# Kernel optimization log

Hardware: AMD Instinct MI355X
Metric: run time of the kernel (lower is better)

Reference implementation:

```python
import jax, jax.numpy as jnp
import numpy as np

BATCH, D_IN, D_HIDDEN, K = 4096, 2048, 16384, 64


def setup_inputs() -> dict:
    key = jax.random.key(0)
    kx, kw = jax.random.split(key)
    x = jax.random.normal(kx, (BATCH, D_IN), dtype=jnp.float32)
    # W init as in the module: randn normalized per column (dim=0) then scaled by 0.1
    W = jax.random.normal(kw, (D_IN, D_HIDDEN), dtype=jnp.float32)
    W = 0.1 * W / jnp.linalg.norm(W, axis=0, keepdims=True)
    b_enc = jnp.zeros((D_HIDDEN,), dtype=jnp.float32)
    b_dec = jnp.zeros((D_IN,), dtype=jnp.float32)
    return {"x": x, "W": W, "b_enc": b_enc, "b_dec": b_dec, "k": K}


def reference(x, W, b_enc, b_dec, k):
    # encode: linear + ReLU
    f = jax.nn.relu(x @ W + b_enc)            # [B, D_HIDDEN]
    # global batch top-k: keep k * batch largest activations across the whole batch
    flat = f.reshape(-1)                      # [B * D_HIDDEN]
    n_keep = k * x.shape[0]                   # static python int
    vals, idx = jax.lax.top_k(flat, n_keep)
    f_topk = jnp.zeros_like(flat).at[idx].set(vals).reshape(f.shape)
    # tied decode
    recon = f_topk @ W.T + b_dec              # [B, D_IN]
    return (recon, f_topk)
```

## Files before the change

### kernel.cpp

```cpp
#include <hip/hip_runtime.h>
#include <stdint.h>


#define BATCH 4096
#define DIN   2048
#define DHID  16384
#define NELEM (BATCH * DHID)
#define RECON_ELEMS (BATCH * DIN)
#define NBINS 8192
#define THRESH_BIN 1664
#define SC_THRESH 0.203125f
#define WIN   3
#define RLCAP 256
#define CBUF2 512
#define NB2 (NBINS - THRESH_BIN)
#define NB2H (NB2 / 2)
#define SCHUNK 32
#define NCH ((NB2 + SCHUNK - 1) / SCHUNK)
#define NKT 32
#define SBUF8 4096
#define WSCALE_INV 0.00390625f

#define XB_OFF   0u
#define HIST_OFF 16777216u
#define META_OFF (HIST_OFF + 32768u)
#define CAND_OFF (HIST_OFF + 65536u)
#define CANDCAP  80000u
#define SC_OFF   18874368u
#define SCCAP    1835008u

#define M_CNT   0
#define M_BLO   1
#define M_BHI   2
#define M_NNEED 3
#define M_NSURE 4
#define M_OVF   5
#define M_SCCNT 6

struct Cand { unsigned long long key; unsigned int idx; float val; };

typedef _Float16 f16x8 __attribute__((ext_vector_type(8)));
typedef float f32x4  __attribute__((ext_vector_type(4)));

__device__ __forceinline__ int binof(float v) {
    int b = (int)(v * 8192.0f);
    return b > (NBINS - 1) ? (NBINS - 1) : b;
}

__device__ __forceinline__ unsigned short f2h(float f) {
    _Float16 h = (_Float16)f;
    return __builtin_bit_cast(unsigned short, h);
}

__device__ __forceinline__ float h2f(unsigned short u) {
    return (float)__builtin_bit_cast(_Float16, u);
}

__device__ __forceinline__ void gload_lds16(const void* g, void* l) {
    __builtin_amdgcn_global_load_lds(
        (const __attribute__((address_space(1))) void*)g,
        (__attribute__((address_space(3))) void*)l, 16, 0, 0);
}

__device__ __forceinline__ void nt_store4(const float4& v, float* p) {
    f32x4 x = {v.x, v.y, v.z, v.w};
    __builtin_nontemporal_store(x, (f32x4*)p);
}

__global__ void init_kernel(unsigned* __restrict__ hist, unsigned* __restrict__ meta) {
    int i = blockIdx.x * 256 + threadIdx.x;
    if (i < NBINS) hist[i] = 0u;
    if (i < 64)    meta[i] = 0u;
}

__global__ __launch_bounds__(256) void convert_x_init(const float* __restrict__ X,
                                                      unsigned short* __restrict__ Xh,
                                                      unsigned* __restrict__ hist,
                                                      unsigned* __restrict__ meta,
                                                      unsigned* __restrict__ rowcnt) {
    const int bid = blockIdx.x;
    size_t i = (size_t)bid * 256 + threadIdx.x;
    float4 v = ((const float4*)X)[i];
    ushort4 o;
    o.x = f2h(v.x); o.y = f2h(v.y); o.z = f2h(v.z); o.w = f2h(v.w);
    ((ushort4*)Xh)[i] = o;
    if (bid < 32) {
        int g = bid * 256 + threadIdx.x;
        if (g < NBINS)  hist[g] = 0u;
        if (g < 64)     meta[g] = 0u;
        if (g < BATCH)  rowcnt[g] = 0u;
    }
}

__global__ __launch_bounds__(256) void transpose_both(const float* __restrict__ W,
                                                      float* __restrict__ WT,
                                                      unsigned short* __restrict__ WhT) {
    __shared__ float tile[64][68];
    const int t  = threadIdx.x;
    const int gx = blockIdx.x;
    const int gy = blockIdx.y;
    const int ra = t >> 4;
    const int ca = (t & 15) * 4;
#pragma unroll
    for (int u = 0; u < 4; ++u) {
        int row = u * 16 + ra;
        float4 v = *(const float4*)&W[(size_t)(gy * 64 + row) * DHID + gx * 64 + ca];
        tile[ca + 0][row] = v.x;
        tile[ca + 1][row] = v.y;
        tile[ca + 2][row] = v.z;
        tile[ca + 3][row] = v.w;
    }
    __syncthreads();
#pragma unroll
    for (int u = 0; u < 4; ++u) {
        int cl = u * 16 + ra;
        float4 v = *(const float4*)&tile[cl][ca];
        size_t o = (size_t)(gx * 64 + cl) * DIN + gy * 64 + ca;
        *(float4*)&WT[o] = v;
        ushort4 b;
        b.x = f2h(v.x * 256.0f); b.y = f2h(v.y * 256.0f);
        b.z = f2h(v.z * 256.0f); b.w = f2h(v.w * 256.0f);
        *(ushort4*)&WhT[o] = b;
    }
}


#define STAGE_A(H, KT) do { if ((KT) < NKT) {                                   \
    const unsigned short* _s = Xh + (size_t)(m0 + (H)*128 + stgrow)*2048        \
                               + (KT)*64 + stgcol;                              \
    unsigned short* _d = lds + ((H)*2 + ((KT)&1))*8192 + stgdst;                \
    gload_lds16(_s, _d);                                                        \
    gload_lds16(_s + 64*2048, _d + 4096);                                       \
} } while (0)

#define STAGE_B(H, KT) do { if ((KT) < NKT) {                                   \
    const unsigned short* _s = WhT + (size_t)(n0 + (H)*128 + stgrow)*2048       \
                               + (KT)*64 + stgcol;                              \
    unsigned short* _d = lds + 32768 + ((H)*2 + ((KT)&1))*8192 + stgdst;        \
    gload_lds16(_s, _d);                                                        \
    gload_lds16(_s + 64*2048, _d + 4096);                                       \
} } while (0)

#define PHASE(Q, PAR, AH, BH, ...) do {                                         \
    f16x8 av[4][2], bv[2][2];                                                   \
    _Pragma("unroll")                                                           \
    for (int i = 0; i < 4; ++i) {                                               \
        const unsigned short* _p = lds + ((AH)*2+(PAR))*8192                    \
                                   + (wr2*64 + i*16 + lm)*64;                   \
        av[i][0] = *(const f16x8*)(_p + cs0);                                   \
        av[i][1] = *(const f16x8*)(_p + cs1);                                   \
    }                                                                           \
    _Pragma("unroll")                                                           \
    for (int j = 0; j < 2; ++j) {                                               \
        const unsigned short* _p = lds + 32768 + ((BH)*2+(PAR))*8192            \
                                   + (wn*32 + j*16 + lm)*64;                    \
        bv[j][0] = *(const f16x8*)(_p + cs0);                                   \
        bv[j][1] = *(const f16x8*)(_p + cs1);                                   \
    }                                                                           \
    __VA_ARGS__                                                                 \
    __builtin_amdgcn_s_barrier();                                               \
    asm volatile("s_waitcnt lgkmcnt(0)" ::: "memory");                          \
    __builtin_amdgcn_sched_barrier(0);                                          \
    __builtin_amdgcn_s_setprio(1);                                              \
    _Pragma("unroll")                                                           \
    for (int i = 0; i < 4; ++i)                                                 \
    _Pragma("unroll")                                                           \
    for (int j = 0; j < 2; ++j) {                                               \
        acc[Q][i][j] = __builtin_amdgcn_mfma_f32_16x16x32_f16(                  \
            av[i][0], bv[j][0], acc[Q][i][j], 0, 0, 0);                         \
        acc[Q][i][j] = __builtin_amdgcn_mfma_f32_16x16x32_f16(                  \
            av[i][1], bv[j][1], acc[Q][i][j], 0, 0, 0);                         \
    }                                                                           \
    __builtin_amdgcn_s_setprio(0);                                              \
    __builtin_amdgcn_s_barrier();                                               \
    asm volatile("" ::: "memory");                                              \
} while (0)

__global__ __launch_bounds__(512, 2) void encode_mfma8(const unsigned short* __restrict__ Xh,
                                                       const unsigned short* __restrict__ WhT,
                                                       const float* __restrict__ benc,
                                                       unsigned long long* __restrict__ sc,
                                                       unsigned* __restrict__ meta,
                                                       unsigned* __restrict__ hist,
                                                       float* __restrict__ F) {
    __shared__ unsigned short lds[65536];
    __shared__ unsigned hsh[NB2H];
    __shared__ unsigned s_n, s_base;

    const int t   = threadIdx.x;
    const int wid = t >> 6;
    const int l   = t & 63;
    const int wr2 = wid >> 2;
    const int wn  = wid & 3;
    const int lm  = l & 15;
    const int l7  = l & 7;
    const int cs0 = ((l >> 4) * 8) ^ (l7 * 8);
    const int cs1 = cs0 ^ 32;
    const int stgrow = wid * 8 + (l >> 3);
    const int stgcol = (l7 ^ (l >> 3)) * 8;
    const int stgdst = wid * 512;

    if (t == 0) s_n = 0u;
    for (int i2 = t; i2 < NB2H; i2 += 512) hsh[i2] = 0u;

    const unsigned id  = blockIdx.x;
    const unsigned xcd = id & 7u;
    const unsigned c   = id >> 3;
    const int bx = (int)(xcd * 8u + (c & 7u));
    const int by = (int)(c >> 3);
    const int m0 = by * 256;
    const int n0 = bx * 256;

    f32x4 acc[4][4][2];
#pragma unroll
    for (int q = 0; q < 4; ++q)
#pragma unroll
        for (int i = 0; i < 4; ++i)
#pragma unroll
            for (int j = 0; j < 2; ++j) acc[q][i][j] = (f32x4){0.f, 0.f, 0.f, 0.f};

    STAGE_A(0, 0); STAGE_B(0, 0); STAGE_B(1, 0); STAGE_A(1, 0);
    STAGE_A(0, 1); STAGE_B(1, 1);
    asm volatile("s_waitcnt vmcnt(4)" ::: "memory");
    __builtin_amdgcn_s_barrier();
    asm volatile("" ::: "memory");

#pragma unroll 1
    for (int it = 0; it < 16; ++it) {
        const int T = 2 * it;
        PHASE(0, 0, 0, 0, STAGE_B(0, T + 1); STAGE_A(1, T + 1););
        PHASE(1, 0, 0, 1, (void)0;);
        PHASE(2, 0, 1, 1, STAGE_A(0, T + 2););
        PHASE(3, 0, 1, 0, STAGE_B(1, T + 2);
                          asm volatile("s_waitcnt vmcnt(4)" ::: "memory"););
        PHASE(0, 1, 0, 0, STAGE_B(0, T + 2); STAGE_A(1, T + 2););
        PHASE(1, 1, 0, 1, (void)0;);
        PHASE(2, 1, 1, 1, STAGE_A(0, T + 3););
        PHASE(3, 1, 1, 0, STAGE_B(1, T + 3);
                          asm volatile("s_waitcnt vmcnt(4)" ::: "memory"););
    }

    __syncthreads();
    unsigned long long* sbuf = (unsigned long long*)lds;

#pragma unroll
    for (int q = 0; q < 4; ++q) {
        const int qm = (q >= 2) ? 1 : 0;
        const int qn = (q == 1 || q == 2) ? 1 : 0;
#pragma unroll
        for (int j = 0; j < 2; ++j) {
            const int col = n0 + qn * 128 + wn * 32 + j * 16 + lm;
            const float bias = benc[col];
#pragma unroll
            for (int i = 0; i < 4; ++i) {
                const int rbase = m0 + qm * 128 + wr2 * 64 + i * 16 + (l >> 4) * 4;
#pragma unroll
                for (int r = 0; r < 4; ++r) {
                    float v = fmaxf(acc[q][i][j][r] * WSCALE_INV + bias, 0.0f);
                    if (v >= SC_THRESH) {
                        unsigned hx = (unsigned)(binof(v) - THRESH_BIN);
                        atomicAdd(&hsh[hx >> 1], (hx & 1u) ? 65536u : 1u);
                        unsigned flat = (unsigned)(rbase + r) * (unsigned)DHID + (unsigned)col;
                        unsigned long long e =
                            ((unsigned long long)__float_as_uint(v) << 32) | flat;
                        unsigned pos = atomicAdd(&s_n, 1u);
                        if (pos < SBUF8) sbuf[pos] = e;
                        else {
                            unsigned p = atomicAdd(&meta[M_SCCNT], 1u);
                            if (p < SCCAP) sc[p] = e; else meta[M_OVF] = 1u;
                        }
                    }
                }
            }
        }
    }
    {
        const float4 z4 = {0.f, 0.f, 0.f, 0.f};
        const int zr = t >> 6;
        const int zc = (t & 63) * 4;
#pragma unroll 1
        for (int rr = 0; rr < 32; ++rr)
            nt_store4(z4, &F[(size_t)(m0 + zr + rr * 8) * DHID + n0 + zc]);
    }
    __syncthreads();
    unsigned n = s_n < SBUF8 ? s_n : (unsigned)SBUF8;
    if (t == 0) s_base = atomicAdd(&meta[M_SCCNT], n);
    __syncthreads();
    const unsigned base = s_base;
    for (unsigned l2 = t; l2 < n; l2 += 512) {
        unsigned p = base + l2;
        if (p < SCCAP) sc[p] = sbuf[l2]; else meta[M_OVF] = 1u;
    }
    for (int i2 = t; i2 < NB2H; i2 += 512) {
        unsigned u = hsh[i2];
        unsigned lo = u & 0xFFFFu, hi = u >> 16;
        if (lo) atomicAdd(&hist[THRESH_BIN + 2 * i2], lo);
        if (hi) atomicAdd(&hist[THRESH_BIN + 2 * i2 + 1], hi);
    }
}

__global__ void scan_sc(const unsigned* __restrict__ hist,
                        unsigned* __restrict__ meta,
                        const int* __restrict__ kptr) {
    __shared__ unsigned sh[NB2];
    __shared__ unsigned csum[NCH];
    int t = threadIdx.x;
    for (int i = t; i < NB2; i += 256) sh[i] = hist[THRESH_BIN + i];
    __syncthreads();
    if (t < NCH) {
        unsigned s = 0;
        int base = t * SCHUNK;
        for (int u = 0; u < SCHUNK && base + u < NB2; ++u) s += sh[base + u];
        csum[t] = s;
    }
    __syncthreads();
    if (t == 0) {
        unsigned nk = (unsigned)kptr[0] * BATCH;
        unsigned cum = 0;
        int bstar_idx = -1;
        for (int c = NCH - 1; c >= 0; --c) {
            if (cum + csum[c] >= nk) {
                int hi2 = c * SCHUNK + SCHUNK - 1; if (hi2 >= NB2) hi2 = NB2 - 1;
                for (int idx = hi2; idx >= c * SCHUNK; --idx) {
                    cum += sh[idx];
                    if (cum >= nk) { bstar_idx = idx; break; }
                }
                break;
            } else cum += csum[c];
        }
        if (bstar_idx < 0) { meta[M_OVF] = 2u; bstar_idx = WIN; }
        int bstar = THRESH_BIN + bstar_idx;
        int blo = bstar - WIN;
        if (blo < THRESH_BIN) { meta[M_OVF] = 3u; blo = THRESH_BIN; }
        int bhi = bstar + WIN; if (bhi > NBINS - 1) bhi = NBINS - 1;
        int bhi_idx = bhi - THRESH_BIN;
        unsigned nsure = 0;
        int cstart = (bhi_idx + 1 + SCHUNK - 1) / SCHUNK;
        for (int idx = bhi_idx + 1; idx < cstart * SCHUNK && idx < NB2; ++idx) nsure += sh[idx];
        for (int c = cstart; c < NCH; ++c) nsure += csum[c];
        meta[M_BLO]   = (unsigned)blo;
        meta[M_BHI]   = (unsigned)bhi;
        meta[M_NSURE] = nsure;
        meta[M_NNEED] = nk - nsure;
    }
}

__global__ __launch_bounds__(256) void emit_sc(const unsigned long long* __restrict__ sc,
                                               unsigned* __restrict__ meta,
                                               Cand* __restrict__ cand,
                                               unsigned* __restrict__ rowcnt,
                                               unsigned long long* __restrict__ rowlist) {
    __shared__ uint2 s_cand[CBUF2];
    __shared__ unsigned s_nc, s_base;
    const int tid = threadIdx.x;
    if (tid == 0) s_nc = 0u;
    __syncthreads();
    const unsigned blo = meta[M_BLO], bhi = meta[M_BHI];
    unsigned C = meta[M_SCCNT]; if (C > SCCAP) C = SCCAP;
    size_t stride = (size_t)gridDim.x * 256;
    for (size_t i = (size_t)blockIdx.x * 256 + tid; i < C; i += stride) {
        unsigned long long e = sc[i];
        unsigned vbits = (unsigned)(e >> 32);
        unsigned idx   = (unsigned)(e & 0xFFFFFFFFu);
        unsigned b = (unsigned)binof(__uint_as_float(vbits));
        if (b > bhi) {
            unsigned row = idx >> 14;
            unsigned pos = atomicAdd(&rowcnt[row], 1u);
            if (pos < RLCAP)
                rowlist[(size_t)row * RLCAP + pos] =
                    ((unsigned long long)vbits << 32) | (idx & (DHID - 1));
            else meta[M_OVF] = 1u;
        } else if (b >= blo) {
            unsigned pos = atomicAdd(&s_nc, 1u);
            if (pos < CBUF2) { s_cand[pos].x = idx; s_cand[pos].y = vbits; }
            else {
                unsigned p = atomicAdd(&meta[M_CNT], 1u);
                if (p < CANDCAP) { cand[p].idx = idx; cand[p].val = __uint_as_float(vbits); }
                else meta[M_OVF] = 1u;
            }
        }
    }
    __syncthreads();
    unsigned nc = s_nc < CBUF2 ? s_nc : (unsigned)CBUF2;
    if (tid == 0) s_base = atomicAdd(&meta[M_CNT], nc);
    __syncthreads();
    const unsigned base = s_base;
    for (unsigned l2 = tid; l2 < nc; l2 += 256) {
        unsigned p = base + l2;
        if (p < CANDCAP) { cand[p].idx = s_cand[l2].x; cand[p].val = __uint_as_float(s_cand[l2].y); }
        else meta[M_OVF] = 1u;
    }
}

__global__ __launch_bounds__(64) void scatter_rl(const unsigned long long* __restrict__ rowlist,
                                                 const unsigned* __restrict__ rowcnt,
                                                 float* __restrict__ F) {
    int b = blockIdx.x;
    unsigned cnt = rowcnt[b]; if (cnt > RLCAP) cnt = RLCAP;
    for (unsigned l = threadIdx.x; l < cnt; l += 64) {
        unsigned long long e = rowlist[(size_t)b * RLCAP + l];
        unsigned j = (unsigned)(e & 0xFFFFFFFFu);
        F[(size_t)b * DHID + j] = __uint_as_float((unsigned)(e >> 32));
    }
}

__global__ __launch_bounds__(256) void exact_wave(const float* __restrict__ X,
                                                  const float* __restrict__ WT,
                                                  const float* __restrict__ benc,
                                                  const unsigned* __restrict__ meta,
                                                  Cand* __restrict__ cand) {
    unsigned C = meta[M_CNT]; if (C > CANDCAP) C = CANDCAP;
    const int lane = threadIdx.x & 63;
    const unsigned wid = blockIdx.x * 4 + (threadIdx.x >> 6);
    const unsigned nw  = gridDim.x * 4;
    for (unsigned c = wid * 2; c < C; c += nw * 2) {
        unsigned c1 = c + 1;
        bool has1 = (c1 < C);
        unsigned idxA = cand[c].idx;
        unsigned idxB = cand[has1 ? c1 : c].idx;
        const float4* xA = (const float4*)(X  + (size_t)(idxA >> 14) * DIN);
        const float4* wA = (const float4*)(WT + (size_t)(idxA & (DHID - 1)) * DIN);
        const float4* xB = (const float4*)(X  + (size_t)(idxB >> 14) * DIN);
        const float4* wB = (const float4*)(WT + (size_t)(idxB & (DHID - 1)) * DIN);
        double a0 = 0.0, a1 = 0.0;
#pragma unroll
        for (int u = 0; u < 8; ++u) {
            float4 xa = xA[lane + 64 * u];
            float4 wa = wA[lane + 64 * u];
            float4 xb = xB[lane + 64 * u];
            float4 wb = wB[lane + 64 * u];
            a0 += (double)xa.x * (double)wa.x + (double)xa.y * (double)wa.y
                + (double)xa.z * (double)wa.z + (double)xa.w * (double)wa.w;
            a1 += (double)xb.x * (double)wb.x + (double)xb.y * (double)wb.y
                + (double)xb.z * (double)wb.z + (double)xb.w * (double)wb.w;
        }
#pragma unroll
        for (int off = 32; off > 0; off >>= 1) {
            a0 += __shfl_down(a0, off, 64);
            a1 += __shfl_down(a1, off, 64);
        }
        if (lane == 0) {
            double v0 = a0 + (double)benc[idxA & (DHID - 1)];
            if (v0 < 0.0) v0 = 0.0;
            cand[c].key = (unsigned long long)__double_as_longlong(v0);
            if (has1) {
                double v1 = a1 + (double)benc[idxB & (DHID - 1)];
                if (v1 < 0.0) v1 = 0.0;
                cand[c1].key = (unsigned long long)__double_as_longlong(v1);
            }
        }
    }
}

__global__ __launch_bounds__(1024) void select_kernel(unsigned* __restrict__ meta,
                                                      Cand* __restrict__ cand) {
    __shared__ unsigned h[4096];
    __shared__ unsigned csum[128];
    __shared__ unsigned long long s_prefix;
    __shared__ unsigned s_need, s_gcnt;
    __shared__ unsigned long long gkey[1024];
    __shared__ unsigned gpos[1024];
    __shared__ unsigned gidx[1024];
    __shared__ unsigned char gkeep[1024];

    int t = threadIdx.x;
    unsigned C = meta[M_CNT]; if (C > CANDCAP) C = CANDCAP;
    if (t == 0) { s_prefix = 0ULL; s_need = meta[M_NNEED]; s_gcnt = 0u; }
    __syncthreads();

    for (int pass = 0; pass < 3; ++pass) {
        for (int i = t; i < 4096; i += 1024) h[i] = 0u;
        __syncthreads();
        int shift = 52 - pass * 12;
        unsigned long long pfx = s_prefix;
        for (unsigned c = t; c < C; c += 1024) {
            unsigned long long key = cand[c].key;
            if (pass == 0 || (key >> (shift + 12)) == pfx)
                atomicAdd(&h[(unsigned)((key >> shift) & 0xFFFULL)], 1u);
        }
        __syncthreads();
        if (t < 128) {
            unsigned s = 0;
#pragma unroll
            for (int u = 0; u < 32; ++u) s += h[t * 32 + u];
            csum[t] = s;
        }
        __syncthreads();
        if (t == 0) {
            unsigned need = s_need;
            unsigned cum2 = 0; int cc = 127;
            for (; cc >= 0; --cc) {
                if (cum2 + csum[cc] >= need) break;
                cum2 += csum[cc];
            }
            int bsel = 0;
            if (cc >= 0) {
                unsigned cum3 = cum2;
                for (int b = cc * 32 + 31; b >= cc * 32; --b) {
                    cum3 += h[b];
                    if (cum3 >= need) { bsel = b; s_need = need - (cum3 - h[b]); break; }
                }
            }
            s_prefix = (s_prefix << 12) | (unsigned long long)bsel;
        }
        __syncthreads();
    }
    unsigned long long pfx = s_prefix;
    for (unsigned c = t; c < C; c += 1024) {
        unsigned long long key = cand[c].key;
        if ((key >> 28) == pfx) {
            unsigned p = atomicAdd(&s_gcnt, 1u);
            if (p < 1024) { gkey[p] = key; gpos[p] = c; gidx[p] = cand[c].idx; gkeep[p] = 0; }
        }
    }
    __syncthreads();
    if (t == 0) {
        unsigned g = s_gcnt < 1024u ? s_gcnt : 1024u;
        unsigned nd = s_need;
        for (unsigned sel = 0; sel < nd && sel < g; ++sel) {
            int best = -1;
            for (unsigned i = 0; i < g; ++i) {
                if (gkeep[i]) continue;
                if (best < 0 || gkey[i] > gkey[best] ||
                    (gkey[i] == gkey[best] && gidx[i] < gidx[best])) best = (int)i;
            }
            if (best >= 0) gkeep[best] = 1;
        }
        for (unsigned i = 0; i < g; ++i)
            if (gkeep[i]) cand[gpos[i]].idx = gidx[i] | 0x80000000u;
    }
    __syncthreads();
    for (unsigned c = t; c < C; c += 1024)
        if ((cand[c].key >> 28) > pfx) cand[c].idx |= 0x80000000u;
}

__global__ __launch_bounds__(256) void restore2_kernel(float* __restrict__ F,
                                                       const unsigned* __restrict__ meta,
                                                       const Cand* __restrict__ cand,
                                                       unsigned* __restrict__ rowcnt,
                                                       unsigned long long* __restrict__ rowlist) {
    unsigned C = meta[M_CNT]; if (C > CANDCAP) C = CANDCAP;
    size_t stride = (size_t)gridDim.x * 256;
    for (size_t c = (size_t)blockIdx.x * 256 + threadIdx.x; c < C; c += stride) {
        unsigned id = cand[c].idx;
        if (id & 0x80000000u) {
            unsigned idx = id & 0x7FFFFFFFu;
            float v = (float)__longlong_as_double((long long)cand[c].key);
            F[idx] = v;
            unsigned row = idx >> 14;
            unsigned j   = idx & (DHID - 1);
            unsigned pos = atomicAdd(&rowcnt[row], 1u);
            if (pos < RLCAP)
                rowlist[(size_t)row * RLCAP + pos] =
                    ((unsigned long long)__float_as_uint(v) << 32) | j;
        }
    }
}

__global__ __launch_bounds__(256) void decode_rl_f32(const unsigned long long* __restrict__ rowlist,
                                                     const unsigned* __restrict__ rowcnt,
                                                     const float* __restrict__ WT,
                                                     const float* __restrict__ bdec,
                                                     float* __restrict__ recon) {
    __shared__ unsigned sj[RLCAP];
    __shared__ float    sv[RLCAP];
    int b = blockIdx.x;
    int t = threadIdx.x;
    unsigned cnt = rowcnt[b]; if (cnt > RLCAP) cnt = RLCAP;
    for (unsigned l = t; l < cnt; l += 256) {
        unsigned long long e = rowlist[(size_t)b * RLCAP + l];
        sj[l] = (unsigned)(e & 0xFFFFFFFFu);
        sv[l] = __uint_as_float((unsigned)(e >> 32));
    }
    __syncthreads();
    float4 acc0 = {0, 0, 0, 0}, acc1 = {0, 0, 0, 0};
    for (unsigned l = 0; l < cnt; ++l) {
        float v = sv[l]; unsigned j = sj[l];
        const float4* w4 = (const float4*)(WT + (size_t)j * DIN);
        float4 wa = w4[t], wb = w4[256 + t];
        acc0.x = fmaf(v, wa.x, acc0.x); acc0.y = fmaf(v, wa.y, acc0.y);
        acc0.z = fmaf(v, wa.z, acc0.z); acc0.w = fmaf(v, wa.w, acc0.w);
        acc1.x = fmaf(v, wb.x, acc1.x); acc1.y = fmaf(v, wb.y, acc1.y);
        acc1.z = fmaf(v, wb.z, acc1.z); acc1.w = fmaf(v, wb.w, acc1.w);
    }
    float4 bd0 = ((const float4*)bdec)[t];
    float4 bd1 = ((const float4*)bdec)[256 + t];
    float4 o0 = {acc0.x + bd0.x, acc0.y + bd0.y, acc0.z + bd0.z, acc0.w + bd0.w};
    float4 o1 = {acc1.x + bd1.x, acc1.y + bd1.y, acc1.z + bd1.z, acc1.w + bd1.w};
    float* dst = recon + (size_t)b * DIN;
    nt_store4(o0, dst + 4 * t);
    nt_store4(o1, dst + 4 * (256 + t));
}

__global__ __launch_bounds__(256) void decode_rl_f16(const unsigned long long* __restrict__ rowlist,
                                                     const unsigned* __restrict__ rowcnt,
                                                     const unsigned short* __restrict__ WhT,
                                                     const float* __restrict__ bdec,
                                                     float* __restrict__ recon) {
    __shared__ unsigned sj[RLCAP];
    __shared__ float    sv[RLCAP];
    int b = blockIdx.x;
    int t = threadIdx.x;
    unsigned cnt = rowcnt[b]; if (cnt > RLCAP) cnt = RLCAP;
    for (unsigned l = t; l < cnt; l += 256) {
        unsigned long long e = rowlist[(size_t)b * RLCAP + l];
        sj[l] = (unsigned)(e & 0xFFFFFFFFu);
        sv[l] = __uint_as_float((unsigned)(e >> 32)) * WSCALE_INV;
    }
    __syncthreads();
    float4 acc0 = {0, 0, 0, 0}, acc1 = {0, 0, 0, 0};
    unsigned l = 0;
    for (; l + 2 <= cnt; l += 2) {
        float v0 = sv[l], v1 = sv[l + 1];
        const ushort4* w0 = (const ushort4*)(WhT + (size_t)sj[l]     * DIN);
        const ushort4* w1 = (const ushort4*)(WhT + (size_t)sj[l + 1] * DIN);
        ushort4 a0 = w0[t], b0 = w0[256 + t];
        ushort4 a1 = w1[t], b1 = w1[256 + t];
        acc0.x = fmaf(v0, h2f(a0.x), acc0.x); acc0.y = fmaf(v0, h2f(a0.y), acc0.y);
        acc0.z = fmaf(v0, h2f(a0.z), acc0.z); acc0.w = fmaf(v0, h2f(a0.w), acc0.w);
        acc1.x = fmaf(v0, h2f(b0.x), acc1.x); acc1.y = fmaf(v0, h2f(b0.y), acc1.y);
        acc1.z = fmaf(v0, h2f(b0.z), acc1.z); acc1.w = fmaf(v0, h2f(b0.w), acc1.w);
        acc0.x = fmaf(v1, h2f(a1.x), acc0.x); acc0.y = fmaf(v1, h2f(a1.y), acc0.y);
        acc0.z = fmaf(v1, h2f(a1.z), acc0.z); acc0.w = fmaf(v1, h2f(a1.w), acc0.w);
        acc1.x = fmaf(v1, h2f(b1.x), acc1.x); acc1.y = fmaf(v1, h2f(b1.y), acc1.y);
        acc1.z = fmaf(v1, h2f(b1.z), acc1.z); acc1.w = fmaf(v1, h2f(b1.w), acc1.w);
    }
    if (l < cnt) {
        float v0 = sv[l];
        const ushort4* w0 = (const ushort4*)(WhT + (size_t)sj[l] * DIN);
        ushort4 a0 = w0[t], b0 = w0[256 + t];
        acc0.x = fmaf(v0, h2f(a0.x), acc0.x); acc0.y = fmaf(v0, h2f(a0.y), acc0.y);
        acc0.z = fmaf(v0, h2f(a0.z), acc0.z); acc0.w = fmaf(v0, h2f(a0.w), acc0.w);
        acc1.x = fmaf(v0, h2f(b0.x), acc1.x); acc1.y = fmaf(v0, h2f(b0.y), acc1.y);
        acc1.z = fmaf(v0, h2f(b0.z), acc1.z); acc1.w = fmaf(v0, h2f(b0.w), acc1.w);
    }
    float4 bd0 = ((const float4*)bdec)[t];
    float4 bd1 = ((const float4*)bdec)[256 + t];
    float4 o0 = {acc0.x + bd0.x, acc0.y + bd0.y, acc0.z + bd0.z, acc0.w + bd0.w};
    float4 o1 = {acc1.x + bd1.x, acc1.y + bd1.y, acc1.z + bd1.z, acc1.w + bd1.w};
    float* dst = recon + (size_t)b * DIN;
    nt_store4(o0, dst + 4 * t);
    nt_store4(o1, dst + 4 * (256 + t));
}

__global__ __launch_bounds__(256) void encode_f32(const float* __restrict__ X,
                                                  const float* __restrict__ W,
                                                  const float* __restrict__ benc,
                                                  float* __restrict__ F) {
    __shared__ float As[16][128];
    __shared__ float Bs[16][128];
    const int t  = threadIdx.x;
    const int n0 = blockIdx.x * 128;
    const int m0 = blockIdx.y * 128;
    const int tx = t & 15, ty = t >> 4;
    const int ra = t >> 1, ca = (t & 1) * 8;
    const int rb = t >> 4, cb = (t & 15) * 8;
    float acc[8][8];
#pragma unroll
    for (int i = 0; i < 8; ++i)
#pragma unroll
        for (int j = 0; j < 8; ++j) acc[i][j] = 0.0f;
    const float* xp = X + (size_t)(m0 + ra) * DIN + ca;
    const float* wp = W + (size_t)rb * DHID + n0 + cb;
    for (int k0 = 0; k0 < DIN; k0 += 16) {
        float4 a0 = *(const float4*)(xp + k0);
        float4 a1 = *(const float4*)(xp + k0 + 4);
        float4 b0 = *(const float4*)(wp + (size_t)k0 * DHID);
        float4 b1 = *(const float4*)(wp + (size_t)k0 * DHID + 4);
        __syncthreads();
        As[ca + 0][ra] = a0.x; As[ca + 1][ra] = a0.y; As[ca + 2][ra] = a0.z; As[ca + 3][ra] = a0.w;
        As[ca + 4][ra] = a1.x; As[ca + 5][ra] = a1.y; As[ca + 6][ra] = a1.z; As[ca + 7][ra] = a1.w;
        *(float4*)&Bs[rb][cb]     = b0;
        *(float4*)&Bs[rb][cb + 4] = b1;
        __syncthreads();
#pragma unroll
        for (int kk = 0; kk < 16; ++kk) {
            float a[8], bb[8];
            *(float4*)&a[0]  = *(const float4*)&As[kk][ty * 8];
            *(float4*)&a[4]  = *(const float4*)&As[kk][ty * 8 + 4];
            *(float4*)&bb[0] = *(const float4*)&Bs[kk][tx * 8];
            *(float4*)&bb[4] = *(const float4*)&Bs[kk][tx * 8 + 4];
#pragma unroll
            for (int i = 0; i < 8; ++i)
#pragma unroll
                for (int j = 0; j < 8; ++j)
                    acc[i][j] = fmaf(a[i], bb[j], acc[i][j]);
        }
    }
    float bias[8];
    *(float4*)&bias[0] = *(const float4*)&benc[n0 + tx * 8];
    *(float4*)&bias[4] = *(const float4*)&benc[n0 + tx * 8 + 4];
#pragma unroll
    for (int i = 0; i < 8; ++i) {
        float out[8];
#pragma unroll
        for (int j = 0; j < 8; ++j) out[j] = fmaxf(acc[i][j] + bias[j], 0.0f);
        float* dst = F + (size_t)(m0 + ty * 8 + i) * DHID + n0 + tx * 8;
        *(float4*)dst       = *(float4*)&out[0];
        *(float4*)(dst + 4) = *(float4*)&out[4];
    }
}

__global__ __launch_bounds__(256) void survey_kernel(const float* __restrict__ F,
                                                     unsigned* __restrict__ hist) {
    __shared__ unsigned h[NBINS];
    for (int i = THRESH_BIN + threadIdx.x; i < NBINS; i += 256) h[i] = 0u;
    __syncthreads();
    const float4* F4 = (const float4*)F;
    size_t stride = (size_t)gridDim.x * 256;
    for (size_t i = (size_t)blockIdx.x * 256 + threadIdx.x; i < NELEM / 4; i += stride) {
        float4 v = F4[i];
        float vv[4] = {v.x, v.y, v.z, v.w};
#pragma unroll
        for (int c = 0; c < 4; ++c) {
            int b = binof(vv[c]);
            if (b >= THRESH_BIN) atomicAdd(&h[b], 1u);
        }
    }
    __syncthreads();
    for (int i2 = THRESH_BIN + threadIdx.x; i2 < NBINS; i2 += 256)
        if (h[i2]) atomicAdd(&hist[i2], h[i2]);
}

__global__ __launch_bounds__(256) void collect_old(const float* __restrict__ F,
                                                   unsigned* __restrict__ meta,
                                                   Cand* __restrict__ cand, unsigned cap) {
    unsigned blo = meta[M_BLO], bhi = meta[M_BHI];
    const float4* F4 = (const float4*)F;
    size_t stride = (size_t)gridDim.x * 256;
    for (size_t i = (size_t)blockIdx.x * 256 + threadIdx.x; i < NELEM / 4; i += stride) {
        float4 v = F4[i];
        float vv[4] = {v.x, v.y, v.z, v.w};
#pragma unroll
        for (int c = 0; c < 4; ++c) {
            unsigned b = (unsigned)binof(vv[c]);
            if (b >= blo && b <= bhi) {
                unsigned p = atomicAdd(&meta[M_CNT], 1u);
                if (p < cap) { cand[p].idx = (unsigned)(i * 4 + c); cand[p].val = vv[c]; }
                else meta[M_OVF] = 1u;
            }
        }
    }
}

__global__ __launch_bounds__(256) void zero_old(float* __restrict__ F,
                                                const unsigned* __restrict__ meta) {
    unsigned bhi = meta[M_BHI];
    float4* F4 = (float4*)F;
    size_t stride = (size_t)gridDim.x * 256;
    for (size_t i = (size_t)blockIdx.x * 256 + threadIdx.x; i < NELEM / 4; i += stride) {
        float4 v = F4[i];
        v.x = ((unsigned)binof(v.x) > bhi) ? v.x : 0.0f;
        v.y = ((unsigned)binof(v.y) > bhi) ? v.y : 0.0f;
        v.z = ((unsigned)binof(v.z) > bhi) ? v.z : 0.0f;
        v.w = ((unsigned)binof(v.w) > bhi) ? v.w : 0.0f;
        F4[i] = v;
    }
}

__global__ __launch_bounds__(256) void exact_old(const float* __restrict__ X,
                                                 const float* __restrict__ W,
                                                 const float* __restrict__ benc,
                                                 const unsigned* __restrict__ meta,
                                                 Cand* __restrict__ cand, unsigned cap) {
    __shared__ double red[256];
    unsigned C = meta[M_CNT]; if (C > cap) C = cap;
    int t = threadIdx.x;
    for (unsigned c = blockIdx.x; c < C; c += gridDim.x) {
        unsigned idx = cand[c].idx;
        int b = (int)(idx >> 14);
        int j = (int)(idx & (DHID - 1));
        const float* xp = X + (size_t)b * DIN + t * 8;
        const float* wp = W + (size_t)(t * 8) * DHID + j;
        double part = 0.0;
#pragma unroll
        for (int u = 0; u < 8; ++u)
            part += (double)xp[u] * (double)wp[(size_t)u * DHID];
        red[t] = part;
        __syncthreads();
        for (int s = 128; s > 0; s >>= 1) {
            if (t < s) red[t] += red[t + s];
            __syncthreads();
        }
        if (t == 0) {
            double v = red[0] + (double)benc[j];
            if (v < 0.0) v = 0.0;
            cand[c].key = (unsigned long long)__double_as_longlong(v);
        }
        __syncthreads();
    }
}

__global__ __launch_bounds__(256) void restore_old(float* __restrict__ F,
                                                   const unsigned* __restrict__ meta,
                                                   const Cand* __restrict__ cand, unsigned cap) {
    unsigned C = meta[M_CNT]; if (C > cap) C = cap;
    size_t stride = (size_t)gridDim.x * 256;
    for (size_t c = (size_t)blockIdx.x * 256 + threadIdx.x; c < C; c += stride) {
        unsigned id = cand[c].idx;
        if (id & 0x80000000u)
            F[id & 0x7FFFFFFFu] = (float)__longlong_as_double((long long)cand[c].key);
    }
}

__global__ __launch_bounds__(256) void decode_old(const float* __restrict__ F,
                                                  const float* __restrict__ W,
                                                  const float* __restrict__ bdec,
                                                  float* __restrict__ recon) {
    __shared__ unsigned sj[4096];
    __shared__ float    sv[4096];
    __shared__ unsigned soff[257];
    int b = blockIdx.x;
    int t = threadIdx.x;
    float4 acc0 = {0, 0, 0, 0}, acc1 = {0, 0, 0, 0};
    const float* frow = F + (size_t)b * DHID;
    for (int seg = 0; seg < 4; ++seg) {
        int base = seg * 4096;
        unsigned cnt = 0;
#pragma unroll
        for (int c = 0; c < 16; ++c)
            if (frow[base + t * 16 + c] != 0.0f) cnt++;
        soff[t] = cnt;
        __syncthreads();
        if (t == 0) {
            unsigned o = 0;
            for (int i = 0; i < 256; ++i) { unsigned tmp = soff[i]; soff[i] = o; o += tmp; }
            soff[256] = o;
        }
        __syncthreads();
        unsigned pos = soff[t];
        for (int c = 0; c < 16; ++c) {
            float v = frow[base + t * 16 + c];
            if (v != 0.0f) { sj[pos] = (unsigned)(base + t * 16 + c); sv[pos] = v; ++pos; }
        }
        __syncthreads();
        unsigned total = soff[256];
        int i0 = t * 4, i1 = 1024 + t * 4;
        for (unsigned l = 0; l < total; ++l) {
            float v = sv[l]; unsigned j = sj[l];
            const float* wp = W + j;
            acc0.x = fmaf(v, wp[(size_t)(i0 + 0) * DHID], acc0.x);
            acc0.y = fmaf(v, wp[(size_t)(i0 + 1) * DHID], acc0.y);
            acc0.z = fmaf(v, wp[(size_t)(i0 + 2) * DHID], acc0.z);
            acc0.w = fmaf(v, wp[(size_t)(i0 + 3) * DHID], acc0.w);
            acc1.x = fmaf(v, wp[(size_t)(i1 + 0) * DHID], acc1.x);
            acc1.y = fmaf(v, wp[(size_t)(i1 + 1) * DHID], acc1.y);
            acc1.z = fmaf(v, wp[(size_t)(i1 + 2) * DHID], acc1.z);
            acc1.w = fmaf(v, wp[(size_t)(i1 + 3) * DHID], acc1.w);
        }
        __syncthreads();
    }
    float4 bd0 = ((const float4*)bdec)[t];
    float4 bd1 = ((const float4*)bdec)[256 + t];
    float4 o0 = {acc0.x + bd0.x, acc0.y + bd0.y, acc0.z + bd0.z, acc0.w + bd0.w};
    float4 o1 = {acc1.x + bd1.x, acc1.y + bd1.y, acc1.z + bd1.z, acc1.w + bd1.w};
    float4* dst = (float4*)(recon + (size_t)b * DIN);
    dst[t]       = o0;
    dst[256 + t] = o1;
}

extern "C" void kernel_launch(void* const* d_in, const int* in_sizes, int n_in,
                              void* d_out, int out_size, void* d_ws, size_t ws_size,
                              hipStream_t stream) {
    const float* X    = (const float*)d_in[0];
    const float* W    = (const float*)d_in[1];
    const float* benc = (const float*)d_in[2];
    const float* bdec = (const float*)d_in[3];
    const int*   kptr = (const int*)d_in[4];

    float* recon = (float*)d_out;
    float* F     = recon + RECON_ELEMS;

    const size_t WT_BYTES  = (size_t)DIN * DHID * sizeof(float);
    const size_t WHT_BYTES = (size_t)DIN * DHID * sizeof(short);
    const size_t ROW_BYTES = 65536 + (size_t)BATCH * RLCAP * 8;
    float* WT = (float*)d_ws;

    if (ws_size >= WT_BYTES + WHT_BYTES) {
        unsigned short* WhT = (unsigned short*)((char*)d_ws + WT_BYTES);
        int f16_decode = (ws_size >= WT_BYTES + WHT_BYTES + ROW_BYTES) ? 1 : 0;
        char* rowbase = f16_decode ? ((char*)d_ws + WT_BYTES + WHT_BYTES)
                                   : ((char*)WhT);
        unsigned* rowcnt = (unsigned*)rowbase;
        unsigned long long* rowlist = (unsigned long long*)(rowbase + 65536);

        unsigned short* Xh = (unsigned short*)((char*)d_out + XB_OFF);
        unsigned* hist = (unsigned*)((char*)d_out + HIST_OFF);
        unsigned* meta = (unsigned*)((char*)d_out + META_OFF);
        Cand*     cand = (Cand*)((char*)d_out + CAND_OFF);
        unsigned long long* sc = (unsigned long long*)((char*)d_out + SC_OFF);

        convert_x_init<<<dim3(8192), dim3(256), 0, stream>>>(X, Xh, hist, meta, rowcnt);
        transpose_both<<<dim3(256, 32), dim3(256), 0, stream>>>(W, WT, WhT);
        encode_mfma8<<<dim3(1024), dim3(512), 0, stream>>>(Xh, WhT, benc, sc, meta, hist, F);
        scan_sc<<<dim3(1), dim3(256), 0, stream>>>(hist, meta, kptr);
        emit_sc<<<dim3(512), dim3(256), 0, stream>>>(sc, meta, cand, rowcnt, rowlist);
        scatter_rl<<<dim3(4096), dim3(64), 0, stream>>>(rowlist, rowcnt, F);
        exact_wave<<<dim3(4096), dim3(256), 0, stream>>>(X, WT, benc, meta, cand);
        select_kernel<<<dim3(1), dim3(1024), 0, stream>>>(meta, cand);
        restore2_kernel<<<dim3(1024), dim3(256), 0, stream>>>(F, meta, cand, rowcnt, rowlist);
        if (f16_decode)
            decode_rl_f16<<<dim3(4096), dim3(256), 0, stream>>>(rowlist, rowcnt, WhT, bdec, recon);
        else
            decode_rl_f32<<<dim3(4096), dim3(256), 0, stream>>>(rowlist, rowcnt, WT, bdec, recon);
    } else {
        unsigned* hist = (unsigned*)d_out;
        unsigned* meta = hist + NBINS;
        Cand*     cand = (Cand*)((char*)d_out + 65536);
        const unsigned cap = 1000000u;

        init_kernel<<<dim3(33), dim3(256), 0, stream>>>(hist, meta);
        encode_f32<<<dim3(128, 32), dim3(256), 0, stream>>>(X, W, benc, F);
        survey_kernel<<<dim3(2048), dim3(256), 0, stream>>>(F, hist);
        scan_sc<<<dim3(1), dim3(256), 0, stream>>>(hist, meta, kptr);
        collect_old<<<dim3(2048), dim3(256), 0, stream>>>(F, meta, cand, cap);
        exact_old<<<dim3(4096), dim3(256), 0, stream>>>(X, W, benc, meta, cand, cap);
        select_kernel<<<dim3(1), dim3(1024), 0, stream>>>(meta, cand);
        zero_old<<<dim3(2048), dim3(256), 0, stream>>>(F, meta);
        restore_old<<<dim3(1024), dim3(256), 0, stream>>>(F, meta, cand, cap);
        decode_old<<<dim3(4096), dim3(256), 0, stream>>>(F, W, bdec, recon);
    }
}
```

Measured before the change: 722.5 us.

## Merge prep kernels, fold scatter into emit, reuse LDS fragments in encode

Combines the X fp16 conversion/init kernel and the W transpose kernel into one launch split by block index. Folds the scatter of confirmed activations into F directly into emit_sc, which removes the scatter_rl launch and its rowlist re-read. Restructures the MFMA phase loop so A and B register fragments are reused across consecutive phases instead of being reloaded from LDS each time. Together these aim to cut launch overhead, redundant global traffic and LDS reads, at the cost of higher register pressure in the encode kernel.

```diff
diff --git a/kernel.cpp b/kernel.cpp
--- a/kernel.cpp
+++ b/kernel.cpp
@@ -73,32 +73,34 @@
     if (i < 64)    meta[i] = 0u;
 }
 
-__global__ __launch_bounds__(256) void convert_x_init(const float* __restrict__ X,
-                                                      unsigned short* __restrict__ Xh,
-                                                      unsigned* __restrict__ hist,
-                                                      unsigned* __restrict__ meta,
-                                                      unsigned* __restrict__ rowcnt) {
+__global__ __launch_bounds__(256) void prep_kernel(const float* __restrict__ X,
+                                                   unsigned short* __restrict__ Xh,
+                                                   const float* __restrict__ W,
+                                                   float* __restrict__ WT,
+                                                   unsigned short* __restrict__ WhT,
+                                                   unsigned* __restrict__ hist,
+                                                   unsigned* __restrict__ meta,
+                                                   unsigned* __restrict__ rowcnt) {
+    __shared__ float tile[64][68];
     const int bid = blockIdx.x;
-    size_t i = (size_t)bid * 256 + threadIdx.x;
-    float4 v = ((const float4*)X)[i];
-    ushort4 o;
-    o.x = f2h(v.x); o.y = f2h(v.y); o.z = f2h(v.z); o.w = f2h(v.w);
-    ((ushort4*)Xh)[i] = o;
-    if (bid < 32) {
-        int g = bid * 256 + threadIdx.x;
-        if (g < NBINS)  hist[g] = 0u;
-        if (g < 64)     meta[g] = 0u;
-        if (g < BATCH)  rowcnt[g] = 0u;
-    }
-}
-
-__global__ __launch_bounds__(256) void transpose_both(const float* __restrict__ W,
-                                                      float* __restrict__ WT,
-                                                      unsigned short* __restrict__ WhT) {
-    __shared__ float tile[64][68];
-    const int t  = threadIdx.x;
-    const int gx = blockIdx.x;
-    const int gy = blockIdx.y;
+    const int t   = threadIdx.x;
+    if (bid < 8192) {
+        size_t i = (size_t)bid * 256 + t;
+        float4 v = ((const float4*)X)[i];
+        ushort4 o;
+        o.x = f2h(v.x); o.y = f2h(v.y); o.z = f2h(v.z); o.w = f2h(v.w);
+        ((ushort4*)Xh)[i] = o;
+        if (bid < 32) {
+            int g = bid * 256 + t;
+            if (g < NBINS)  hist[g] = 0u;
+            if (g < 64)     meta[g] = 0u;
+            if (g < BATCH)  rowcnt[g] = 0u;
+        }
+        return;
+    }
+    const int bb = bid - 8192;
+    const int gx = bb & 255;
+    const int gy = bb >> 8;
     const int ra = t >> 4;
     const int ca = (t & 15) * 4;
 #pragma unroll
@@ -141,23 +143,27 @@
     gload_lds16(_s + 64*2048, _d + 4096);                                       \
 } } while (0)
 
-#define PHASE(Q, PAR, AH, BH, ...) do {                                         \
-    f16x8 av[4][2], bv[2][2];                                                   \
+#define LDA(DST, AH, PAR) do {                                                  \
     _Pragma("unroll")                                                           \
     for (int i = 0; i < 4; ++i) {                                               \
         const unsigned short* _p = lds + ((AH)*2+(PAR))*8192                    \
                                    + (wr2*64 + i*16 + lm)*64;                   \
-        av[i][0] = *(const f16x8*)(_p + cs0);                                   \
-        av[i][1] = *(const f16x8*)(_p + cs1);                                   \
+        DST[i][0] = *(const f16x8*)(_p + cs0);                                  \
+        DST[i][1] = *(const f16x8*)(_p + cs1);                                  \
     }                                                                           \
+} while (0)
+
+#define LDB(DST, BH, PAR) do {                                                  \
     _Pragma("unroll")                                                           \
     for (int j = 0; j < 2; ++j) {                                               \
         const unsigned short* _p = lds + 32768 + ((BH)*2+(PAR))*8192            \
                                    + (wn*32 + j*16 + lm)*64;                    \
-        bv[j][0] = *(const f16x8*)(_p + cs0);                                   \
-        bv[j][1] = *(const f16x8*)(_p + cs1);                                   \
+        DST[j][0] = *(const f16x8*)(_p + cs0);                                  \
+        DST[j][1] = *(const f16x8*)(_p + cs1);                                  \
     }                                                                           \
-    __VA_ARGS__                                                                 \
+} while (0)
+
+#define DO_MFMA(Q, AV, BV) do {                                                 \
     __builtin_amdgcn_s_barrier();                                               \
     asm volatile("s_waitcnt lgkmcnt(0)" ::: "memory");                          \
     __builtin_amdgcn_sched_barrier(0);                                          \
@@ -167,13 +173,27 @@
     _Pragma("unroll")                                                           \
     for (int j = 0; j < 2; ++j) {                                               \
         acc[Q][i][j] = __builtin_amdgcn_mfma_f32_16x16x32_f16(                  \
-            av[i][0], bv[j][0], acc[Q][i][j], 0, 0, 0);                         \
+            AV[i][0], BV[j][0], acc[Q][i][j], 0, 0, 0);                         \
         acc[Q][i][j] = __builtin_amdgcn_mfma_f32_16x16x32_f16(                  \
-            av[i][1], bv[j][1], acc[Q][i][j], 0, 0, 0);                         \
+            AV[i][1], BV[j][1], acc[Q][i][j], 0, 0, 0);                         \
     }                                                                           \
     __builtin_amdgcn_s_setprio(0);                                              \
     __builtin_amdgcn_s_barrier();                                               \
     asm volatile("" ::: "memory");                                              \
+} while (0)
+
+#define TILE_BODY(PAR, T) do {                                                  \
+    LDA(av, 0, PAR); LDB(bv0, 0, PAR);                                          \
+    STAGE_B(0, (T) + 1); STAGE_A(1, (T) + 1);                                   \
+    DO_MFMA(0, av, bv0);                                                        \
+    LDB(bv1, 1, PAR);                                                           \
+    DO_MFMA(1, av, bv1);                                                        \
+    LDA(av, 1, PAR);                                                            \
+    STAGE_A(0, (T) + 2);                                                        \
+    DO_MFMA(2, av, bv1);                                                        \
+    STAGE_B(1, (T) + 2);                                                        \
+    asm volatile("s_waitcnt vmcnt(4)" ::: "memory");                            \
+    DO_MFMA(3, av, bv0);                                                        \
 } while (0)
 
 __global__ __launch_bounds__(512, 2) void encode_mfma8(const unsigned short* __restrict__ Xh,
@@ -225,19 +245,14 @@
     __builtin_amdgcn_s_barrier();
     asm volatile("" ::: "memory");
 
+    {
+        f16x8 av[4][2], bv0[2][2], bv1[2][2];
 #pragma unroll 1
-    for (int it = 0; it < 16; ++it) {
-        const int T = 2 * it;
-        PHASE(0, 0, 0, 0, STAGE_B(0, T + 1); STAGE_A(1, T + 1););
-        PHASE(1, 0, 0, 1, (void)0;);
-        PHASE(2, 0, 1, 1, STAGE_A(0, T + 2););
-        PHASE(3, 0, 1, 0, STAGE_B(1, T + 2);
-                          asm volatile("s_waitcnt vmcnt(4)" ::: "memory"););
-        PHASE(0, 1, 0, 0, STAGE_B(0, T + 2); STAGE_A(1, T + 2););
-        PHASE(1, 1, 0, 1, (void)0;);
-        PHASE(2, 1, 1, 1, STAGE_A(0, T + 3););
-        PHASE(3, 1, 1, 0, STAGE_B(1, T + 3);
-                          asm volatile("s_waitcnt vmcnt(4)" ::: "memory"););
+        for (int it = 0; it < 16; ++it) {
+            const int T = 2 * it;
+            TILE_BODY(0, T);
+            TILE_BODY(1, T + 1);
+        }
     }
 
     __syncthreads();
@@ -349,7 +364,8 @@
                                                unsigned* __restrict__ meta,
                                                Cand* __restrict__ cand,
                                                unsigned* __restrict__ rowcnt,
-                                               unsigned long long* __restrict__ rowlist) {
+                                               unsigned long long* __restrict__ rowlist,
+                                               float* __restrict__ F) {
     __shared__ uint2 s_cand[CBUF2];
     __shared__ unsigned s_nc, s_base;
     const int tid = threadIdx.x;
@@ -364,6 +380,7 @@
         unsigned idx   = (unsigned)(e & 0xFFFFFFFFu);
         unsigned b = (unsigned)binof(__uint_as_float(vbits));
         if (b > bhi) {
+            F[idx] = __uint_as_float(vbits);
             unsigned row = idx >> 14;
             unsigned pos = atomicAdd(&rowcnt[row], 1u);
             if (pos < RLCAP)
@@ -389,18 +406,6 @@
         unsigned p = base + l2;
         if (p < CANDCAP) { cand[p].idx = s_cand[l2].x; cand[p].val = __uint_as_float(s_cand[l2].y); }
         else meta[M_OVF] = 1u;
-    }
-}
-
-__global__ __launch_bounds__(64) void scatter_rl(const unsigned long long* __restrict__ rowlist,
-                                                 const unsigned* __restrict__ rowcnt,
-                                                 float* __restrict__ F) {
-    int b = blockIdx.x;
-    unsigned cnt = rowcnt[b]; if (cnt > RLCAP) cnt = RLCAP;
-    for (unsigned l = threadIdx.x; l < cnt; l += 64) {
-        unsigned long long e = rowlist[(size_t)b * RLCAP + l];
-        unsigned j = (unsigned)(e & 0xFFFFFFFFu);
-        F[(size_t)b * DHID + j] = __uint_as_float((unsigned)(e >> 32));
     }
 }
 
@@ -890,12 +895,10 @@
         Cand*     cand = (Cand*)((char*)d_out + CAND_OFF);
         unsigned long long* sc = (unsigned long long*)((char*)d_out + SC_OFF);
 
-        convert_x_init<<<dim3(8192), dim3(256), 0, stream>>>(X, Xh, hist, meta, rowcnt);
-        transpose_both<<<dim3(256, 32), dim3(256), 0, stream>>>(W, WT, WhT);
+        prep_kernel<<<dim3(16384), dim3(256), 0, stream>>>(X, Xh, W, WT, WhT, hist, meta, rowcnt);
         encode_mfma8<<<dim3(1024), dim3(512), 0, stream>>>(Xh, WhT, benc, sc, meta, hist, F);
         scan_sc<<<dim3(1), dim3(256), 0, stream>>>(hist, meta, kptr);
-        emit_sc<<<dim3(512), dim3(256), 0, stream>>>(sc, meta, cand, rowcnt, rowlist);
-        scatter_rl<<<dim3(4096), dim3(64), 0, stream>>>(rowlist, rowcnt, F);
+        emit_sc<<<dim3(512), dim3(256), 0, stream>>>(sc, meta, cand, rowcnt, rowlist, F);
         exact_wave<<<dim3(4096), dim3(256), 0, stream>>>(X, WT, benc, meta, cand);
         select_kernel<<<dim3(1), dim3(1024), 0, stream>>>(meta, cand);
         restore2_kernel<<<dim3(1024), dim3(256), 0, stream>>>(F, meta, cand, rowcnt, rowlist);
```

New measurement: 672.8 us, median of 2. 1.07x faster.
